# Kernel optimization log

Measured on AMD Instinct MI355X. Metric: run time of the kernel, lower is better.

The kernel has to match this reference:

```python
import jax, jax.numpy as jnp
import numpy as np
import math

NUM_SEGMENTS = 4      # num_bezier_segments
SHARPNESS = 75.0
SAMPLE_RATE = 16      # curve samples per bezier segment


def _control_radians(S):
    # replicates the __init__ control-polygon angle construction
    theta = math.pi * 2 / (4 * S) + math.atan(math.tan(2 * math.pi / (4 * S)) / 3.0)
    r = []
    for i in range(S):
        base = 2 * math.pi / S * i
        r += [base, base + theta, 2 * math.pi / S * (i + 1) - theta]
    return jnp.asarray(np.asarray(r, dtype=np.float32).reshape(S, 3))


def _quat_rotate_inv(q, p):
    # rotate p (...,3) by the conjugate of quaternion q (...,4), wxyz convention
    q = q / jnp.linalg.norm(q, axis=-1, keepdims=True)
    w = q[..., 0:1]
    v = -q[..., 1:4]
    t = 2.0 * jnp.cross(v, p)
    return p + w * t + jnp.cross(v, t)


def _csg_stump(points, primitive_parameters, iw, uw, is_training):
    pp = jnp.swapaxes(primitive_parameters, 1, 2)          # (B,K,P)
    B, K, P = pp.shape
    S, R = NUM_SEGMENTS, SAMPLE_RATE
    quat = pp[:, :, :4]
    trans = pp[:, :, 4:7]
    height = pp[:, :, 7]                                   # (B,K)
    radius = jnp.abs(pp[:, :, 8:8 + 3 * S].reshape(B, K, S, 3))
    wts = jnp.abs(pp[:, :, 8 + 3 * S:8 + 5 * S].reshape(B, K, S, 2))

    rad = _control_radians(S)                              # (S,3)
    cp = jnp.stack([jnp.cos(rad) * radius, jnp.sin(rad) * radius], axis=-1)  # (B,K,S,3,2)

    # closed rational cubic bezier spline: segment s uses cp[s,0..2] and cp[s+1,0]
    P0, P1, P2 = cp[:, :, :, 0], cp[:, :, :, 1], cp[:, :, :, 2]
    P3 = jnp.roll(P0, -1, axis=2)
    t = jnp.arange(R, dtype=pp.dtype) / R                  # (R,) endpoint-free
    b0 = (1 - t) ** 3; b1 = 3 * t * (1 - t) ** 2; b2 = 3 * t ** 2 * (1 - t); b3 = t ** 3
    w1 = wts[..., 0:1]; w2 = wts[..., 1:2]                 # (B,K,S,1)
    num = (b0[:, None] * P0[..., None, :]
           + (b1[:, None] * w1[..., None]) * P1[..., None, :]
           + (b2[:, None] * w2[..., None]) * P2[..., None, :]
           + b3[:, None] * P3[..., None, :])               # (B,K,S,R,2)
    den = b0 + b1 * w1 + b2 * w2 + b3                       # (B,K,S,R)
    curve = (num / den[..., None]).reshape(B, K, S * R, 2)  # (B,K,N,2)

    # transform query points into each primitive's local frame
    p_loc = _quat_rotate_inv(quat[:, None], points[:, :, None, :] - trans[:, None])  # (B,M,K,3)
    pxy = p_loc[..., :2]
    pz = p_loc[..., 2]

    # point-to-curve distances without materializing the (B,M,K,N,2) diff
    p_sq = jnp.sum(pxy * pxy, axis=-1)                      # (B,M,K)
    c_sq = jnp.sum(curve * curve, axis=-1)                  # (B,K,N)
    dots = jnp.einsum('bmkd,bknd->bmkn', pxy, curve)
    d = jnp.sqrt(jnp.maximum(p_sq[..., None] + c_sq[:, None] - 2.0 * dots, 0.0) + 1e-12)
    ud = jnp.min(d, axis=-1)                                # (B,M,K) unsigned 2D distance
    idx = jnp.argmin(d, axis=-1)
    curve_r = jnp.sqrt(c_sq)                                # (B,K,N)
    r_near = jnp.take_along_axis(jnp.broadcast_to(curve_r[:, None], d.shape),
                                 idx[..., None], axis=-1)[..., 0]
    sign = jax.lax.stop_gradient(jnp.where(jnp.sqrt(p_sq) <= r_near, -1.0, 1.0))
    sdf2d = sign * ud

    # extrusion along z
    dz = jnp.abs(pz) - height[:, None, :]
    primitive_sdf = (jnp.minimum(jnp.maximum(sdf2d, dz), 0.0)
                     + jnp.sqrt(jnp.maximum(sdf2d, 0.0) ** 2 + jnp.maximum(dz, 0.0) ** 2 + 1e-12))
    support_distances = ud

    occ = jax.nn.sigmoid(-primitive_sdf * SHARPNESS)        # (B,M,K)

    # soft intersection: bkc,bmk->bmkc selection
    pre_i = iw[:, None] * occ[..., None] + (1.0 - iw)[:, None]    # (B,M,K,C)
    if is_training:
        w = jax.lax.stop_gradient(jax.nn.softmax(pre_i * -40.0, axis=-2))
        inter = jnp.sum(w * pre_i, axis=-2)                 # (B,M,C)
    else:
        inter = jnp.min(pre_i, axis=-2)

    # soft union
    pre_u = uw[:, None, :] * inter                          # (B,M,C)
    if is_training:
        w = jax.lax.stop_gradient(jax.nn.softmax(pre_u * 40.0, axis=-1))
        occupancies = jnp.sum(w * pre_u, axis=-1)           # (B,M)
    else:
        occupancies = jnp.max(pre_u, axis=-1)

    return occupancies, primitive_sdf, inter, support_distances


def setup_inputs() -> dict:
    key = jax.random.key(0)
    k1, k2, k3, k4 = jax.random.split(key, 4)
    B, M, K, C = 4, 8192, 64, 32
    P = 8 + 5 * NUM_SEGMENTS  # 28
    return {
        'sample_point_coordinates': jax.random.uniform(k1, (B, M, 3), dtype=jnp.float32),
        'primitive_parameters': jax.random.normal(k2, (B, P, K), dtype=jnp.float32),
        'intersection_layer_weights': jax.random.uniform(k3, (B, K, C), dtype=jnp.float32),
        'union_layer_weights': jax.random.uniform(k4, (B, C), dtype=jnp.float32),
        'is_training': 1,
    }


def reference(sample_point_coordinates, primitive_parameters, intersection_layer_weights,
              union_layer_weights, is_training):
    return _csg_stump(sample_point_coordinates, primitive_parameters,
                      intersection_layer_weights, union_layer_weights, bool(is_training))
```

## Files before the change

kernel.cpp:

```cpp
#include <hip/hip_runtime.h>
#include <math.h>

#define Bb 4
#define Mm 8192
#define Kk 64
#define Cc 32
#define Pp 28

#define OFF_PSDF  (Bb*Mm)
#define OFF_INTER (Bb*Mm + Bb*Mm*Kk)
#define OFF_SD    (Bb*Mm + Bb*Mm*Kk + Bb*Mm*Cc)

#define W40    57.707801635558535f
#define NL2_40 (-0.017328679513998632f)
#define S75    108.20212806667225f
#define EPS_OCC 1e-6f

struct Rad12 { float v[12]; };

__device__ __forceinline__ float fexp2(float x){ return __builtin_amdgcn_exp2f(x); }
__device__ __forceinline__ float frcp(float x){ return __builtin_amdgcn_rcpf(x); }

__global__ __launch_bounds__(256)
void curve_prep(const float* __restrict__ pp, const float* __restrict__ iw_g,
                Rad12 rad,
                float* __restrict__ ws_c, float* __restrict__ params_ws,
                float2* __restrict__ st_ws)
{
    const int g = blockIdx.x * 256 + threadIdx.x;
    const int k = g & 63;
    const int n = (g >> 6) & 63;
    const int b = g >> 12;

#define PP(p) pp[((b * Pp) + (p)) * Kk + k]

    const int s  = n >> 4;
    const int it = n & 15;
    const float t = (float)it * 0.0625f;
    const int s1 = (s + 1) & 3;

    float r0 = fabsf(PP(8 + 3 * s + 0));
    float r1 = fabsf(PP(8 + 3 * s + 1));
    float r2 = fabsf(PP(8 + 3 * s + 2));
    float r3 = fabsf(PP(8 + 3 * s1 + 0));
    float w1 = fabsf(PP(20 + 2 * s + 0));
    float w2 = fabsf(PP(20 + 2 * s + 1));

    float a0 = rad.v[3 * s + 0], a1 = rad.v[3 * s + 1];
    float a2 = rad.v[3 * s + 2], a3 = rad.v[3 * s1 + 0];

    float P0x = cosf(a0) * r0, P0y = sinf(a0) * r0;
    float P1x = cosf(a1) * r1, P1y = sinf(a1) * r1;
    float P2x = cosf(a2) * r2, P2y = sinf(a2) * r2;
    float P3x = cosf(a3) * r3, P3y = sinf(a3) * r3;

    float omt = 1.0f - t;
    float b0 = omt * omt * omt;
    float b1 = (3.0f * t) * (omt * omt);
    float b2 = (3.0f * (t * t)) * omt;
    float b3 = t * t * t;
    float bw1 = b1 * w1, bw2 = b2 * w2;
    float den = ((b0 + bw1) + bw2) + b3;
    float nx  = ((b0 * P0x + bw1 * P1x) + bw2 * P2x) + b3 * P3x;
    float ny  = ((b0 * P0y + bw1 * P1y) + bw2 * P2y) + b3 * P3y;

    float cx = nx / den, cy = ny / den;
    const int j = n >> 1, h = n & 1;
    float* base = ws_c + (((b * 32 + j) * 64) + k) * 4;
    base[h]     = -2.0f * cx;
    base[2 + h] = -2.0f * cy;

    if (n < 8) {
        float val;
        if (n < 4) {
            float q0 = PP(0), q1 = PP(1), q2 = PP(2), q3 = PP(3);
            float nrm = sqrtf(q0 * q0 + q1 * q1 + q2 * q2 + q3 * q3);
            val = PP(n) / nrm;
        } else {
            val = PP(n);
        }
        params_ws[(b * Kk + k) * 8 + n] = val;
    }
#undef PP

    if (blockIdx.x == 0 && threadIdx.x < 128) {
        const int tb = threadIdx.x >> 5, tc = threadIdx.x & 31;
        float S = 0.0f, T = 0.0f;
        for (int kk = 0; kk < 64; ++kk) {
            float w   = iw_g[tb * 2048 + kk * 32 + tc];
            float b40 = (w - 1.0f) * W40;
            float e   = fexp2(b40);
            S += e;
            T  = fmaf(e, b40, T);
        }
        st_ws[threadIdx.x] = make_float2(S, T);
    }
}

__global__ __launch_bounds__(512)
void csg_main(const float* __restrict__ pts, const float* __restrict__ iw_g,
              const float* __restrict__ uw_g, const int* __restrict__ flag,
              const float* __restrict__ ws_c, const float* __restrict__ params_ws,
              const float2* __restrict__ st_ws, float* __restrict__ out)
{
    __shared__ __align__(16) float s_pool[8192];

    const int tid = threadIdx.x;
    const int bid = blockIdx.x;
    const int b   = bid >> 8;
    const int m0  = (bid & 255) << 5;

    float wreg[4];
    {
        const float4* cs = (const float4*)(ws_c + (size_t)b * 8192);
        float4* cd = (float4*)s_pool;
#pragma unroll
        for (int i = 0; i < 4; ++i) cd[tid + i * 512] = cs[tid + i * 512];
#pragma unroll
        for (int i = 0; i < 4; ++i) wreg[i] = iw_g[b * 2048 + tid + i * 512];
    }
    __syncthreads();

    const int wid  = tid >> 6;
    const int lane = tid & 63;
    const int k    = lane;
    const int pt0  = b * Mm + m0 + (wid << 2);

    const float4* prm4 = (const float4*)(params_ws + ((b << 6) + k) * 8);
    float4 q4 = prm4[0];
    float4 t4 = prm4[1];

    const float4* pts4 = (const float4*)(pts + (size_t)pt0 * 3);
    float4 A = pts4[0], Bv = pts4[1], Cv = pts4[2];
    float pxs[4] = {A.x, A.w, Bv.z, Cv.y};
    float pys[4] = {A.y, Bv.x, Bv.w, Cv.z};
    float pzs[4] = {A.z, Bv.y, Cv.x, Cv.w};

    float px4[4], py4[4], plzv[4], psq[4];
    {
        float vx = -q4.y, vy = -q4.z, vz = -q4.w, qw = q4.x;
#pragma unroll
        for (int p = 0; p < 4; ++p) {
            float px = pxs[p] - t4.x, py = pys[p] - t4.y, pz = pzs[p] - t4.z;
            float t1x = 2.0f * (vy * pz - vz * py);
            float t1y = 2.0f * (vz * px - vx * pz);
            float t1z = 2.0f * (vx * py - vy * px);
            float plx = px + qw * t1x + (vy * t1z - vz * t1y);
            float ply = py + qw * t1y + (vz * t1x - vx * t1z);
            plzv[p] = pz + qw * t1z + (vx * t1y - vy * t1x);
            psq[p]  = plx * plx + ply * ply;
            px4[p]  = 4.0f * plx;
            py4[p]  = 4.0f * ply;
        }
    }

    float best4[4] = {1e30f, 1e30f, 1e30f, 1e30f};
    float bcsq4[4] = {0.0f, 0.0f, 0.0f, 0.0f};
    {
        const float4* cdp = (const float4*)&s_pool[k * 4];
#pragma unroll 4
        for (int j = 0; j < 32; ++j) {
            float4 cd = cdp[j * 64];
            float cq4x = fmaf(cd.x, cd.x, cd.z * cd.z);
            float cq4y = fmaf(cd.y, cd.y, cd.w * cd.w);
#pragma unroll
            for (int p = 0; p < 4; ++p) {
                float da = fmaf(cd.x, px4[p], fmaf(cd.z, py4[p], cq4x));
                if (da < best4[p]) { best4[p] = da; bcsq4[p] = cq4x; }
                float db = fmaf(cd.y, px4[p], fmaf(cd.w, py4[p], cq4y));
                if (db < best4[p]) { best4[p] = db; bcsq4[p] = cq4y; }
            }
        }
    }

    float occ[4];
    unsigned long long mask[4];
#pragma unroll
    for (int p = 0; p < 4; ++p) {
        float d2    = psq[p] + 0.25f * best4[p];
        float bq    = 0.25f * bcsq4[p];
        float ud    = sqrtf(fmaxf(d2, 0.0f) + 1e-12f);
        float sgn   = (psq[p] <= bq) ? -1.0f : 1.0f;
        float sdf2d = sgn * ud;
        float dzv   = fabsf(plzv[p]) - t4.w;
        float inner = fminf(fmaxf(sdf2d, dzv), 0.0f);
        float r1m   = fmaxf(sdf2d, 0.0f), r2m = fmaxf(dzv, 0.0f);
        float psdf  = inner + sqrtf(r1m * r1m + r2m * r2m + 1e-12f);
        out[OFF_PSDF + (pt0 + p) * Kk + k] = psdf;
        out[OFF_SD   + (pt0 + p) * Kk + k] = ud;
        occ[p]  = frcp(1.0f + fexp2(S75 * psdf));
        mask[p] = __ballot(occ[p] > EPS_OCC);
    }

    const int c = lane & 31;
    float2 s0t0 = st_ws[b * 32 + c];

    __syncthreads();
    {
        const int ptl = wid << 2;
#pragma unroll
        for (int p = 0; p < 4; ++p)
            s_pool[(ptl + p) * 64 + k] = occ[p];
#pragma unroll
        for (int i = 0; i < 4; ++i) {
            int idx = tid + i * 512;
            float w = wreg[i];
            ((float2*)&s_pool[2048])[idx] = make_float2(w * (-W40), (w - 1.0f) * W40);
        }
    }
    __syncthreads();

    const int training = flag[0];
    const float2* tbl = (const float2*)&s_pool[2048];

    float inter[4];
    if (training) {
#pragma unroll
        for (int p = 0; p < 4; ++p) {
            unsigned long long m = mask[p];
            const int ptl = (wid << 2) + p;
            float sw = s0t0.x, swp = s0t0.y;
            while (m) {
                int kk = __builtin_ctzll(m); m &= m - 1;
                float osv = s_pool[ptl * 64 + kk];
                float2 wv = tbl[kk * 32 + c];
                float pre = fmaf(wv.x, osv, wv.y);
                float e   = fexp2(pre);
                float e0  = fexp2(wv.y);
                sw  += (e - e0);
                swp += fmaf(e, pre, -(e0 * wv.y));
            }
            inter[p] = swp * frcp(sw) * NL2_40;
        }
    } else {
#pragma unroll
        for (int p = 0; p < 4; ++p) {
            const int ptl = (wid << 2) + p;
            float mx = -1e30f;
#pragma unroll 8
            for (int kk = 0; kk < 64; ++kk) {
                float osv = s_pool[ptl * 64 + kk];
                float2 wv = tbl[kk * 32 + c];
                mx = fmaxf(mx, fmaf(wv.x, osv, wv.y));
            }
            inter[p] = mx * NL2_40;
        }
    }

    if (lane < Cc) {
#pragma unroll
        for (int p = 0; p < 4; ++p)
            out[OFF_INTER + (pt0 + p) * Cc + c] = inter[p];
    }

    float uwv = uw_g[b * Cc + c];
    float resv[4];
    if (training) {
#pragma unroll
        for (int p = 0; p < 4; ++p) {
            float pu  = uwv * inter[p];
            float e   = fexp2(W40 * pu);
            float num = e * pu, den = e;
#pragma unroll
            for (int msk = 16; msk >= 1; msk >>= 1) {
                num += __shfl_xor(num, msk, 64);
                den += __shfl_xor(den, msk, 64);
            }
            resv[p] = num * frcp(den);
        }
    } else {
#pragma unroll
        for (int p = 0; p < 4; ++p) {
            float pu = uwv * inter[p];
#pragma unroll
            for (int msk = 16; msk >= 1; msk >>= 1)
                pu = fmaxf(pu, __shfl_xor(pu, msk, 64));
            resv[p] = pu;
        }
    }
    if (lane == 0)
        *(float4*)(out + pt0) = make_float4(resv[0], resv[1], resv[2], resv[3]);
}

extern "C" void kernel_launch(void* const* d_in, const int* in_sizes, int n_in,
                              void* d_out, int out_size, void* d_ws, size_t ws_size,
                              hipStream_t stream)
{
    const float* pts  = (const float*)d_in[0];
    const float* pp   = (const float*)d_in[1];
    const float* iw   = (const float*)d_in[2];
    const float* uw   = (const float*)d_in[3];
    const int*   flag = (const int*)d_in[4];
    float* out = (float*)d_out;

    float*  ws_c   = (float*)d_ws;
    float*  params = ws_c + 32768;
    float2* st_ws  = (float2*)(params + 2048);

    Rad12 rad;
    const double th = M_PI * 2.0 / 16.0 + atan(tan(2.0 * M_PI / 16.0) / 3.0);
    for (int i = 0; i < 4; ++i) {
        double base = 2.0 * M_PI / 4.0 * (double)i;
        rad.v[3 * i + 0] = (float)base;
        rad.v[3 * i + 1] = (float)(base + th);
        rad.v[3 * i + 2] = (float)(2.0 * M_PI / 4.0 * (double)(i + 1) - th);
    }

    curve_prep<<<64, 256, 0, stream>>>(pp, iw, rad, ws_c, params, st_ws);
    csg_main<<<Bb * Mm / 32, 512, 0, stream>>>(pts, iw, uw, flag,
                                               ws_c, params, st_ws, out);
}
```

Baseline: 40.34 us.

## Merge per-point sparse masks and batch four points per primitive iteration

Replaces the four per-point ballot masks with one union mask and loops once over active primitives, handling all four points per iteration. Occupancies are stored transposed with a padded stride so one float4 LDS read fetches four points' values, and the weight table is loaded and its exp2 computed once instead of four times. The cost is evaluating primitives that are active for only some of the four points; those extra terms cancel to zero because e equals e0 when occupancy is zero. The LDS layout change also shifts the table offset.

```diff
diff --git a/kernel.cpp b/kernel.cpp
--- a/kernel.cpp
+++ b/kernel.cpp
@@ -15,6 +15,9 @@
 #define NL2_40 (-0.017328679513998632f)
 #define S75    108.20212806667225f
 #define EPS_OCC 1e-6f
+
+#define OCC_STRIDE 36
+#define TBL_OFF    2304
 
 struct Rad12 { float v[12]; };
 
@@ -174,7 +177,7 @@
     }
 
     float occ[4];
-    unsigned long long mask[4];
+    unsigned long long mu = 0ull;
 #pragma unroll
     for (int p = 0; p < 4; ++p) {
         float d2    = psq[p] + 0.25f * best4[p];
@@ -189,7 +192,7 @@
         out[OFF_PSDF + (pt0 + p) * Kk + k] = psdf;
         out[OFF_SD   + (pt0 + p) * Kk + k] = ud;
         occ[p]  = frcp(1.0f + fexp2(S75 * psdf));
-        mask[p] = __ballot(occ[p] > EPS_OCC);
+        mu |= __ballot(occ[p] > EPS_OCC);
     }
 
     const int c = lane & 31;
@@ -197,54 +200,58 @@
 
     __syncthreads();
     {
-        const int ptl = wid << 2;
-#pragma unroll
-        for (int p = 0; p < 4; ++p)
-            s_pool[(ptl + p) * 64 + k] = occ[p];
+        *(float4*)&s_pool[k * OCC_STRIDE + (wid << 2)] =
+            make_float4(occ[0], occ[1], occ[2], occ[3]);
 #pragma unroll
         for (int i = 0; i < 4; ++i) {
             int idx = tid + i * 512;
             float w = wreg[i];
-            ((float2*)&s_pool[2048])[idx] = make_float2(w * (-W40), (w - 1.0f) * W40);
+            ((float2*)&s_pool[TBL_OFF])[idx] = make_float2(w * (-W40), (w - 1.0f) * W40);
         }
     }
     __syncthreads();
 
     const int training = flag[0];
-    const float2* tbl = (const float2*)&s_pool[2048];
+    const float2* tbl = (const float2*)&s_pool[TBL_OFF];
+    const int ows = wid << 2;
 
     float inter[4];
     if (training) {
-#pragma unroll
-        for (int p = 0; p < 4; ++p) {
-            unsigned long long m = mask[p];
-            const int ptl = (wid << 2) + p;
-            float sw = s0t0.x, swp = s0t0.y;
-            while (m) {
-                int kk = __builtin_ctzll(m); m &= m - 1;
-                float osv = s_pool[ptl * 64 + kk];
-                float2 wv = tbl[kk * 32 + c];
-                float pre = fmaf(wv.x, osv, wv.y);
+        float sw[4]  = {s0t0.x, s0t0.x, s0t0.x, s0t0.x};
+        float swp[4] = {s0t0.y, s0t0.y, s0t0.y, s0t0.y};
+        unsigned long long m = mu;
+        while (m) {
+            int kk = __builtin_ctzll(m); m &= m - 1;
+            float4 o4 = *(const float4*)&s_pool[kk * OCC_STRIDE + ows];
+            float2 wv = tbl[kk * 32 + c];
+            float e0  = fexp2(wv.y);
+            float e0b = e0 * wv.y;
+            float os[4] = {o4.x, o4.y, o4.z, o4.w};
+#pragma unroll
+            for (int p = 0; p < 4; ++p) {
+                float pre = fmaf(wv.x, os[p], wv.y);
                 float e   = fexp2(pre);
-                float e0  = fexp2(wv.y);
-                sw  += (e - e0);
-                swp += fmaf(e, pre, -(e0 * wv.y));
+                sw[p]  += (e - e0);
+                swp[p] += fmaf(e, pre, -e0b);
             }
-            inter[p] = swp * frcp(sw) * NL2_40;
-        }
+        }
+#pragma unroll
+        for (int p = 0; p < 4; ++p)
+            inter[p] = swp[p] * frcp(sw[p]) * NL2_40;
     } else {
-#pragma unroll
-        for (int p = 0; p < 4; ++p) {
-            const int ptl = (wid << 2) + p;
-            float mx = -1e30f;
+        float mx[4] = {-1e30f, -1e30f, -1e30f, -1e30f};
 #pragma unroll 8
-            for (int kk = 0; kk < 64; ++kk) {
-                float osv = s_pool[ptl * 64 + kk];
-                float2 wv = tbl[kk * 32 + c];
-                mx = fmaxf(mx, fmaf(wv.x, osv, wv.y));
-            }
-            inter[p] = mx * NL2_40;
-        }
+        for (int kk = 0; kk < 64; ++kk) {
+            float4 o4 = *(const float4*)&s_pool[kk * OCC_STRIDE + ows];
+            float2 wv = tbl[kk * 32 + c];
+            float os[4] = {o4.x, o4.y, o4.z, o4.w};
+#pragma unroll
+            for (int p = 0; p < 4; ++p)
+                mx[p] = fmaxf(mx[p], fmaf(wv.x, os[p], wv.y));
+        }
+#pragma unroll
+        for (int p = 0; p < 4; ++p)
+            inter[p] = mx[p] * NL2_40;
     }
 
     if (lane < Cc) {
```

Result: no change. 40.41 us (+0.2%).
